# Optimization experiments

Hardware: AMD Instinct MI355X
Metric: run time of the kernel (lower is better)

## Reference

```python
import jax, jax.numpy as jnp
import numpy as np

B, T, KV = 128, 400, 128   # batch, encoder length, key/value size
V, E, H = 1024, 256, 512   # vocab, embed dim, decoder hidden dim
L = 300                    # decode length (train mode: y.shape[1])
SOS = 1                    # letter2index['<sos>'] (0 is padding_idx)
NEG = -1e9


def setup_inputs() -> dict:
    key = jax.random.key(0)
    ks = jax.random.split(key, 16)
    s1 = 1.0 / np.sqrt(H)   # torch LSTMCell init scale
    s2 = 1.0 / np.sqrt(KV)
    so = 1.0 / np.sqrt(2 * KV)
    emb = jax.random.normal(ks[4], (V, E), jnp.float32)
    emb = emb.at[0].set(0.0)  # padding_idx=0
    return {
        "enc_key": jax.random.normal(ks[0], (B, T, KV), jnp.float32),
        "enc_value": jax.random.normal(ks[1], (B, T, KV), jnp.float32),
        "encoder_len": jax.random.randint(ks[2], (B,), 1, T + 1),
        "y": jax.random.randint(ks[3], (B, L), 0, V),
        "embedding": emb,
        "w_ih1": jax.random.uniform(ks[5], (4 * H, KV + E), jnp.float32, -s1, s1),
        "w_hh1": jax.random.uniform(ks[6], (4 * H, H), jnp.float32, -s1, s1),
        "b_ih1": jax.random.uniform(ks[7], (4 * H,), jnp.float32, -s1, s1),
        "b_hh1": jax.random.uniform(ks[8], (4 * H,), jnp.float32, -s1, s1),
        "w_ih2": jax.random.uniform(ks[9], (4 * KV, H), jnp.float32, -s2, s2),
        "w_hh2": jax.random.uniform(ks[10], (4 * KV, KV), jnp.float32, -s2, s2),
        "b_ih2": jax.random.uniform(ks[11], (4 * KV,), jnp.float32, -s2, s2),
        "b_hh2": jax.random.uniform(ks[12], (4 * KV,), jnp.float32, -s2, s2),
        "w_out": jax.random.uniform(ks[13], (V, 2 * KV), jnp.float32, -so, so),
        "b_out": jax.random.uniform(ks[14], (V,), jnp.float32, -so, so),
    }


def _lstm_cell(x, h, c, w_ih, w_hh, b_ih, b_hh):
    gates = x @ w_ih.T + b_ih + h @ w_hh.T + b_hh
    i, f, g, o = jnp.split(gates, 4, axis=-1)
    c2 = jax.nn.sigmoid(f) * c + jax.nn.sigmoid(i) * jnp.tanh(g)
    h2 = jax.nn.sigmoid(o) * jnp.tanh(c2)
    return h2, c2


def reference(enc_key, enc_value, encoder_len, y, embedding,
              w_ih1, w_hh1, b_ih1, b_hh1,
              w_ih2, w_hh2, b_ih2, b_hh2,
              w_out, b_out):
    mask = jnp.arange(T)[None, :] < encoder_len[:, None]  # (B, T)

    # Teacher forcing (TF_rate -> 1): step 0 feeds <sos>, step i feeds y[:, i-1]
    char_emb = embedding[y]                               # (B, L, E)
    sos_emb = jnp.broadcast_to(embedding[SOS], (B, E))
    inputs = jnp.concatenate([sos_emb[:, None, :], char_emb[:, :-1, :]], axis=1)
    inputs = jnp.swapaxes(inputs, 0, 1)                   # (L, B, E)

    def step(carry, emb_t):
        h1, c1, h2, c2, context = carry
        x = jnp.concatenate([emb_t, context], axis=1)     # (B, E+KV)
        h1, c1 = _lstm_cell(x, h1, c1, w_ih1, w_hh1, b_ih1, b_hh1)
        h2, c2 = _lstm_cell(h1, h2, c2, w_ih2, w_hh2, b_ih2, b_hh2)
        query = h2                                        # (B, KV)
        energy = jnp.einsum('btd,bd->bt', enc_key, query)
        energy = jnp.where(mask, energy, NEG)
        attn = jax.nn.softmax(energy, axis=1)             # (B, T)
        context = jnp.einsum('bt,btd->bd', attn, enc_value)
        logits = jnp.concatenate([query, context], axis=1) @ w_out.T + b_out
        return (h1, c1, h2, c2, context), (logits, attn[0])

    zH = jnp.zeros((B, H), jnp.float32)
    zK = jnp.zeros((B, KV), jnp.float32)
    carry0 = (zH, zH, zK, zK, zK)
    _, (logits_seq, attn_plot) = jax.lax.scan(step, carry0, inputs)
    predictions = jnp.swapaxes(logits_seq, 0, 1)          # (B, L, V)
    return predictions, attn_plot                         # attn_plot: (L, T)
```

## Files before the change

### kernel.cpp

```cpp
#include <hip/hip_runtime.h>
#include <hip/hip_bf16.h>

#define BB   128
#define TT   400
#define KVD  128
#define VV   1024
#define EE   256
#define HH   512
#define LL   300
#define D1   896
#define NBLK 256
#define NTHR 256

#define XT_SZ   (D1 * BB)
#define XT_OFF  0
#define H2_SZ   (KVD * BB)
#define H2_OFF  (2 * XT_SZ)
#define FLAG_OFF (H2_OFF + 2 * H2_SZ)
#define PLOT_OFF (BB * LL * VV)

typedef unsigned short ushort_t;

__device__ __forceinline__ float bf2f(ushort_t u) {
  return __uint_as_float(((unsigned)u) << 16);
}
__device__ __forceinline__ ushort_t f2bf(float f) {
  unsigned u = __float_as_uint(f);
  return (ushort_t)((u + 0x7FFFu + ((u >> 16) & 1u)) >> 16);
}
__device__ __forceinline__ float sigm(float x) { return 1.0f / (1.0f + expf(-x)); }

__device__ __forceinline__ float ldx(const void* p, size_t i, bool isf) {
  return isf ? ((const float*)p)[i] : bf2f(((const ushort_t*)p)[i]);
}
__device__ __forceinline__ void stx(void* p, size_t i, float v, bool isf) {
  if (isf) ((float*)p)[i] = v; else ((ushort_t*)p)[i] = f2bf(v);
}

__global__ void probe_kernel(const void* __restrict__ w_out, float* __restrict__ ws) {
  if (blockIdx.x == 0 && threadIdx.x == 0) {
    const ushort_t* p = (const ushort_t*)w_out;
    int bad = 0;
    for (int i = 0; i < 512; ++i) {
      float v = bf2f(p[i]);
      if (!(fabsf(v) < 0.5f)) bad++;
    }
    unsigned* flags = (unsigned*)(ws + FLAG_OFF);
    flags[NBLK + 1] = (bad > 0) ? 1u : 0u;
  }
}

__global__ void __launch_bounds__(NTHR) init_kernel(const void* __restrict__ emb,
                                                    float* __restrict__ ws) {
  unsigned* flags = (unsigned*)(ws + FLAG_OFF);
  const bool isf = flags[NBLK + 1] != 0;
  int idx = blockIdx.x * NTHR + threadIdx.x;
  if (idx < XT_SZ) {
    int k = idx >> 7;
    ws[XT_OFF + idx] = (k < EE) ? ldx(emb, EE + k, isf) : 0.0f;
  }
  int j = idx - XT_SZ;
  if (j >= 0 && j < H2_SZ) ws[H2_OFF + j] = 0.0f;
  int f = idx - (XT_SZ + H2_SZ);
  if (f >= 0 && f < NBLK + 1) flags[f] = 0u;
}

__device__ __forceinline__ void grid_barrier(unsigned* flags, unsigned* gen, unsigned target) {
  __syncthreads();
  const int tid = threadIdx.x;
  if (blockIdx.x == 0) {
    if (tid > 0) {
      long spin = 0;
      while (__hip_atomic_load(&flags[tid], __ATOMIC_RELAXED, __HIP_MEMORY_SCOPE_AGENT) < target) {
        __builtin_amdgcn_s_sleep(2);
        if (++spin > (1L << 24)) break;
      }
    }
    __syncthreads();
    if (tid == 0) {
      __threadfence();
      __hip_atomic_store(gen, target, __ATOMIC_RELEASE, __HIP_MEMORY_SCOPE_AGENT);
    }
    __syncthreads();
  } else {
    if (tid == 0) {
      __threadfence();
      __hip_atomic_store(&flags[blockIdx.x], target, __ATOMIC_RELEASE, __HIP_MEMORY_SCOPE_AGENT);
      long spin = 0;
      while (__hip_atomic_load(gen, __ATOMIC_RELAXED, __HIP_MEMORY_SCOPE_AGENT) < target) {
        __builtin_amdgcn_s_sleep(2);
        if (++spin > (1L << 24)) break;
      }
      __threadfence();
    }
    __syncthreads();
  }
}

__global__ void __launch_bounds__(NTHR) decoder_kernel(
    const void* __restrict__ enc_key,
    const void* __restrict__ enc_value,
    const int*  __restrict__ enc_len,
    const int*  __restrict__ y,
    const void* __restrict__ emb,
    const void* __restrict__ w_ih1, const void* __restrict__ w_hh1,
    const void* __restrict__ b_ih1, const void* __restrict__ b_hh1,
    const void* __restrict__ w_ih2, const void* __restrict__ w_hh2,
    const void* __restrict__ b_ih2, const void* __restrict__ b_hh2,
    const void* __restrict__ w_out, const void* __restrict__ b_out,
    void* __restrict__ out, float* __restrict__ ws)
{
  __shared__ float sW1[8][D1];
  __shared__ float sW2[4][640];
  __shared__ float sWo[4][256];
  __shared__ float sB1[8];
  __shared__ float sB2[4];
  __shared__ float sBo[4];
  __shared__ float sRed[4];
  __shared__ float sAttn[TT];
  __shared__ float sH2[KVD];
  __shared__ float sGex[2][BB];

  const int tid = threadIdx.x;
  const int w   = blockIdx.x;
  unsigned* flags = (unsigned*)(ws + FLAG_OFF);
  unsigned* gen   = flags + NBLK;
  const bool isf  = flags[NBLK + 1] != 0;

  for (int i = tid; i < 8 * D1; i += NTHR) {
    int r = i / D1, k = i - r * D1;
    int g = r & 3, h = r >> 2;
    int R = g * HH + 2 * w + h;
    sW1[r][k] = (k < EE + KVD) ? ldx(w_ih1, (size_t)R * (EE + KVD) + k, isf)
                               : ldx(w_hh1, (size_t)R * HH + (k - (EE + KVD)), isf);
  }
  if (tid < 8) {
    int R = (tid & 3) * HH + 2 * w + (tid >> 2);
    sB1[tid] = ldx(b_ih1, R, isf) + ldx(b_hh1, R, isf);
  }
  if (w < BB) {
    for (int i = tid; i < 4 * 640; i += NTHR) {
      int g = i / 640, k = i - g * 640;
      int R = g * KVD + w;
      sW2[g][k] = (k < HH) ? ldx(w_ih2, (size_t)R * HH + k, isf)
                           : ldx(w_hh2, (size_t)R * KVD + (k - HH), isf);
    }
    if (tid < 4) {
      int R = tid * KVD + w;
      sB2[tid] = ldx(b_ih2, R, isf) + ldx(b_hh2, R, isf);
    }
  }
  for (int i = tid; i < 4 * 256; i += NTHR) {
    int r = i >> 8, d = i & 255;
    sWo[r][d] = ldx(w_out, (size_t)(4 * w + r) * 256 + d, isf);
  }
  if (tid < 4) sBo[tid] = ldx(b_out, 4 * w + tid, isf);
  __syncthreads();

  const int b  = tid & 127;
  const int hi = tid >> 7;
  float c1 = 0.0f;
  float c2 = 0.0f;

  unsigned target = 0;

  for (int t = 0; t <= LL; ++t) {
    const int p0 = t & 1;
    float* xT0  = ws + XT_OFF + p0 * XT_SZ;
    float* xT1  = ws + XT_OFF + (p0 ^ 1) * XT_SZ;
    float* h2T0 = ws + H2_OFF + p0 * H2_SZ;
    float* h2T1 = ws + H2_OFF + (p0 ^ 1) * H2_SZ;

    if (t > 0) {
      float a0 = sBo[2 * hi], a1 = sBo[2 * hi + 1];
      const float4* r0 = (const float4*)&sWo[2 * hi][0];
      const float4* r1 = (const float4*)&sWo[2 * hi + 1][0];
      const float* hp = h2T0 + b;
      #pragma unroll 4
      for (int q = 0; q < 32; ++q) {
        float x0 = hp[0], x1 = hp[BB], x2 = hp[2 * BB], x3 = hp[3 * BB]; hp += 4 * BB;
        float4 u0 = r0[q], u1 = r1[q];
        a0 += u0.x * x0 + u0.y * x1 + u0.z * x2 + u0.w * x3;
        a1 += u1.x * x0 + u1.y * x1 + u1.z * x2 + u1.w * x3;
      }
      const float* cp = xT0 + 256 * BB + b;
      #pragma unroll 4
      for (int q = 0; q < 32; ++q) {
        float x0 = cp[0], x1 = cp[BB], x2 = cp[2 * BB], x3 = cp[3 * BB]; cp += 4 * BB;
        float4 u0 = r0[32 + q], u1 = r1[32 + q];
        a0 += u0.x * x0 + u0.y * x1 + u0.z * x2 + u0.w * x3;
        a1 += u1.x * x0 + u1.y * x1 + u1.z * x2 + u1.w * x3;
      }
      int v = 4 * w + 2 * hi;
      size_t oidx = (size_t)b * (LL * VV) + (size_t)(t - 1) * VV + v;
      stx(out, oidx, a0, isf);
      stx(out, oidx + 1, a1, isf);
    }
    if (t == LL) break;

    {
      const int hu = 2 * w + hi;
      float a0 = sB1[4 * hi + 0], a1 = sB1[4 * hi + 1];
      float a2 = sB1[4 * hi + 2], a3 = sB1[4 * hi + 3];
      const float4* q0 = (const float4*)&sW1[4 * hi + 0][0];
      const float4* q1 = (const float4*)&sW1[4 * hi + 1][0];
      const float4* q2 = (const float4*)&sW1[4 * hi + 2][0];
      const float4* q3 = (const float4*)&sW1[4 * hi + 3][0];
      const float* xp = xT0 + b;
      #pragma unroll 2
      for (int q = 0; q < 224; ++q) {
        float x0 = xp[0], x1 = xp[BB], x2 = xp[2 * BB], x3 = xp[3 * BB]; xp += 4 * BB;
        float4 u0 = q0[q], u1 = q1[q], u2 = q2[q], u3 = q3[q];
        a0 += u0.x * x0 + u0.y * x1 + u0.z * x2 + u0.w * x3;
        a1 += u1.x * x0 + u1.y * x1 + u1.z * x2 + u1.w * x3;
        a2 += u2.x * x0 + u2.y * x1 + u2.z * x2 + u2.w * x3;
        a3 += u3.x * x0 + u3.y * x1 + u3.z * x2 + u3.w * x3;
      }
      float ig = sigm(a0), fg = sigm(a1), gg = tanhf(a2), og = sigm(a3);
      c1 = fg * c1 + ig * gg;
      float h1v = og * tanhf(c1);
      xT1[(384 + hu) * BB + b] = h1v;
    }
    grid_barrier(flags, gen, ++target);

    if (w < BB) {
      float a0 = sB2[2 * hi], a1 = sB2[2 * hi + 1];
      const float4* r0 = (const float4*)&sW2[2 * hi][0];
      const float4* r1 = (const float4*)&sW2[2 * hi + 1][0];
      const float* xp = xT1 + 384 * BB + b;
      #pragma unroll 4
      for (int q = 0; q < 128; ++q) {
        float x0 = xp[0], x1 = xp[BB], x2 = xp[2 * BB], x3 = xp[3 * BB]; xp += 4 * BB;
        float4 u0 = r0[q], u1 = r1[q];
        a0 += u0.x * x0 + u0.y * x1 + u0.z * x2 + u0.w * x3;
        a1 += u1.x * x0 + u1.y * x1 + u1.z * x2 + u1.w * x3;
      }
      const float* hp = h2T0 + b;
      #pragma unroll 4
      for (int q = 0; q < 32; ++q) {
        float x0 = hp[0], x1 = hp[BB], x2 = hp[2 * BB], x3 = hp[3 * BB]; hp += 4 * BB;
        float4 u0 = r0[128 + q], u1 = r1[128 + q];
        a0 += u0.x * x0 + u0.y * x1 + u0.z * x2 + u0.w * x3;
        a1 += u1.x * x0 + u1.y * x1 + u1.z * x2 + u1.w * x3;
      }
      if (hi == 1) { sGex[0][b] = tanhf(a0); sGex[1][b] = sigm(a1); }
      __syncthreads();
      if (hi == 0) {
        c2 = sigm(a1) * c2 + sigm(a0) * sGex[0][b];
        float h2v = sGex[1][b] * tanhf(c2);
        h2T1[w * BB + b] = h2v;
      }
    } else {
      int j = w - BB;
      int tok = y[j * LL + t];
      xT1[tid * BB + j] = ldx(emb, (size_t)tok * EE + tid, isf);
    }
    grid_barrier(flags, gen, ++target);

    if (w < BB) {
      const int rb = w;
      if (tid < KVD) sH2[tid] = h2T1[tid * BB + rb];
      __syncthreads();
      const int len = enc_len[rb];
      float lmax = -3.0e38f;
      #pragma unroll
      for (int rep = 0; rep < 2; ++rep) {
        int tp = tid + rep * 256;
        float e = -3.0e38f;
        if (tp < TT) {
          float acc = 0.0f;
          if (isf) {
            const float4* kr = (const float4*)((const float*)enc_key + ((size_t)rb * TT + tp) * KVD);
            #pragma unroll 8
            for (int q = 0; q < 32; ++q) {
              float4 u = kr[q];
              acc += u.x * sH2[4 * q + 0] + u.y * sH2[4 * q + 1]
                   + u.z * sH2[4 * q + 2] + u.w * sH2[4 * q + 3];
            }
          } else {
            const ushort4* kr = (const ushort4*)((const ushort_t*)enc_key + ((size_t)rb * TT + tp) * KVD);
            #pragma unroll 8
            for (int q = 0; q < 32; ++q) {
              ushort4 u = kr[q];
              acc += bf2f(u.x) * sH2[4 * q + 0] + bf2f(u.y) * sH2[4 * q + 1]
                   + bf2f(u.z) * sH2[4 * q + 2] + bf2f(u.w) * sH2[4 * q + 3];
            }
          }
          e = (tp < len) ? acc : -1e9f;
          sAttn[tp] = e;
        }
        lmax = fmaxf(lmax, e);
      }
      for (int off = 32; off > 0; off >>= 1) lmax = fmaxf(lmax, __shfl_down(lmax, off, 64));
      if ((tid & 63) == 0) sRed[tid >> 6] = lmax;
      __syncthreads();
      const float m = fmaxf(fmaxf(sRed[0], sRed[1]), fmaxf(sRed[2], sRed[3]));
      float lsum = 0.0f;
      #pragma unroll
      for (int rep = 0; rep < 2; ++rep) {
        int tp = tid + rep * 256;
        if (tp < TT) { float a = expf(sAttn[tp] - m); sAttn[tp] = a; lsum += a; }
      }
      for (int off = 32; off > 0; off >>= 1) lsum += __shfl_down(lsum, off, 64);
      __syncthreads();
      if ((tid & 63) == 0) sRed[tid >> 6] = lsum;
      __syncthreads();
      const float rS = 1.0f / (sRed[0] + sRed[1] + sRed[2] + sRed[3]);
      #pragma unroll
      for (int rep = 0; rep < 2; ++rep) {
        int tp = tid + rep * 256;
        if (tp < TT) {
          float a = sAttn[tp] * rS;
          sAttn[tp] = a;
          if (rb == 0) stx(out, (size_t)PLOT_OFF + (size_t)t * TT + tp, a, isf);
        }
      }
      __syncthreads();
      {
        const int d = tid & 127, half = tid >> 7;
        float acc = 0.0f;
        if (isf) {
          const float* vc = (const float*)enc_value + ((size_t)rb * TT + half * 200) * KVD + d;
          for (int tp2 = 0; tp2 < 200; ++tp2) acc += sAttn[half * 200 + tp2] * vc[(size_t)tp2 * KVD];
        } else {
          const ushort_t* vc = (const ushort_t*)enc_value + ((size_t)rb * TT + half * 200) * KVD + d;
          for (int tp2 = 0; tp2 < 200; ++tp2) acc += sAttn[half * 200 + tp2] * bf2f(vc[(size_t)tp2 * KVD]);
        }
        if (half == 1) sGex[0][d] = acc;
        __syncthreads();
        if (half == 0) xT1[(256 + d) * BB + rb] = acc + sGex[0][d];
      }
    }
    grid_barrier(flags, gen, ++target);
  }
}

extern "C" void kernel_launch(void* const* d_in, const int* in_sizes, int n_in,
                              void* d_out, int out_size, void* d_ws, size_t ws_size,
                              hipStream_t stream) {
  const void* enc_key   = d_in[0];
  const void* enc_value = d_in[1];
  const int*  enc_len   = (const int*)d_in[2];
  const int*  y         = (const int*)d_in[3];
  const void* emb       = d_in[4];
  const void* w_ih1     = d_in[5];
  const void* w_hh1     = d_in[6];
  const void* b_ih1     = d_in[7];
  const void* b_hh1     = d_in[8];
  const void* w_ih2     = d_in[9];
  const void* w_hh2     = d_in[10];
  const void* b_ih2     = d_in[11];
  const void* b_hh2     = d_in[12];
  const void* w_out     = d_in[13];
  const void* b_out     = d_in[14];
  float* ws = (float*)d_ws;

  probe_kernel<<<dim3(1), dim3(64), 0, stream>>>(w_out, ws);
  init_kernel<<<dim3((XT_SZ + H2_SZ + NBLK + 1 + NTHR - 1) / NTHR), dim3(NTHR), 0, stream>>>(emb, ws);
  decoder_kernel<<<dim3(NBLK), dim3(NTHR), 0, stream>>>(
      enc_key, enc_value, enc_len, y, emb,
      w_ih1, w_hh1, b_ih1, b_hh1,
      w_ih2, w_hh2, b_ih2, b_hh2,
      w_out, b_out, d_out, ws);
}
```

Baseline: 31.83 ms.

## Stage activation chunks through LDS with register prefetch in LSTM and output GEMVs

Replaces the direct strided global reads of the transposed activation vectors (x, h1, h2, context) with a double-step pipeline. Each block cooperatively loads 32-row chunks as coalesced float4 into registers, writes them to a shared buffer, and prefetches the next chunk while computing from LDS. The aim is to cut redundant per-thread global/L2 traffic, since both halves of the block read the same activations, and to hide load latency. In exchange it adds two __syncthreads per chunk and 16KB more shared memory.

```diff
diff --git a/kernel.cpp b/kernel.cpp
--- a/kernel.cpp
+++ b/kernel.cpp
@@ -96,6 +96,27 @@
     __syncthreads();
   }
 }
+
+#define STAGE_LOAD(PF, SRC4, C) \
+  { _Pragma("unroll") for (int j = 0; j < 4; ++j) PF[j] = (SRC4)[(size_t)(C) * 1024 + j * 256 + tid]; }
+#define STAGE_WRITE(PF) \
+  { float4* s4 = (float4*)sX; _Pragma("unroll") for (int j = 0; j < 4; ++j) s4[j * 256 + tid] = PF[j]; }
+#define CHUNK_CP4(WB) \
+  { _Pragma("unroll") for (int q = 0; q < 8; ++q) { \
+      float x0 = sX[(4*q+0)*128 + b], x1 = sX[(4*q+1)*128 + b]; \
+      float x2 = sX[(4*q+2)*128 + b], x3 = sX[(4*q+3)*128 + b]; \
+      float4 u0 = q0[(WB)+q], u1 = q1[(WB)+q], u2 = q2[(WB)+q], u3 = q3[(WB)+q]; \
+      a0 += u0.x*x0 + u0.y*x1 + u0.z*x2 + u0.w*x3; \
+      a1 += u1.x*x0 + u1.y*x1 + u1.z*x2 + u1.w*x3; \
+      a2 += u2.x*x0 + u2.y*x1 + u2.z*x2 + u2.w*x3; \
+      a3 += u3.x*x0 + u3.y*x1 + u3.z*x2 + u3.w*x3; } }
+#define CHUNK_CP2(WB) \
+  { _Pragma("unroll") for (int q = 0; q < 8; ++q) { \
+      float x0 = sX[(4*q+0)*128 + b], x1 = sX[(4*q+1)*128 + b]; \
+      float x2 = sX[(4*q+2)*128 + b], x3 = sX[(4*q+3)*128 + b]; \
+      float4 u0 = r0[(WB)+q], u1 = r1[(WB)+q]; \
+      a0 += u0.x*x0 + u0.y*x1 + u0.z*x2 + u0.w*x3; \
+      a1 += u1.x*x0 + u1.y*x1 + u1.z*x2 + u1.w*x3; } }
 
 __global__ void __launch_bounds__(NTHR) decoder_kernel(
     const void* __restrict__ enc_key,
@@ -120,6 +141,7 @@
   __shared__ float sAttn[TT];
   __shared__ float sH2[KVD];
   __shared__ float sGex[2][BB];
+  __shared__ float sX[32 * 128];
 
   const int tid = threadIdx.x;
   const int w   = blockIdx.x;
@@ -175,21 +197,19 @@
       float a0 = sBo[2 * hi], a1 = sBo[2 * hi + 1];
       const float4* r0 = (const float4*)&sWo[2 * hi][0];
       const float4* r1 = (const float4*)&sWo[2 * hi + 1][0];
-      const float* hp = h2T0 + b;
-      #pragma unroll 4
-      for (int q = 0; q < 32; ++q) {
-        float x0 = hp[0], x1 = hp[BB], x2 = hp[2 * BB], x3 = hp[3 * BB]; hp += 4 * BB;
-        float4 u0 = r0[q], u1 = r1[q];
-        a0 += u0.x * x0 + u0.y * x1 + u0.z * x2 + u0.w * x3;
-        a1 += u1.x * x0 + u1.y * x1 + u1.z * x2 + u1.w * x3;
-      }
-      const float* cp = xT0 + 256 * BB + b;
-      #pragma unroll 4
-      for (int q = 0; q < 32; ++q) {
-        float x0 = cp[0], x1 = cp[BB], x2 = cp[2 * BB], x3 = cp[3 * BB]; cp += 4 * BB;
-        float4 u0 = r0[32 + q], u1 = r1[32 + q];
-        a0 += u0.x * x0 + u0.y * x1 + u0.z * x2 + u0.w * x3;
-        a1 += u1.x * x0 + u1.y * x1 + u1.z * x2 + u1.w * x3;
+      const float4* hsrc = (const float4*)h2T0;
+      const float4* csrc = (const float4*)(xT0 + 256 * BB);
+      float4 pf[4];
+      STAGE_LOAD(pf, hsrc, 0)
+      for (int c = 0; c < 8; ++c) {
+        __syncthreads();
+        STAGE_WRITE(pf)
+        if (c < 7) {
+          if (c < 3) STAGE_LOAD(pf, hsrc, c + 1)
+          else       STAGE_LOAD(pf, csrc, c - 3)
+        }
+        __syncthreads();
+        CHUNK_CP2(c * 8)
       }
       int v = 4 * w + 2 * hi;
       size_t oidx = (size_t)b * (LL * VV) + (size_t)(t - 1) * VV + v;
@@ -206,15 +226,15 @@
       const float4* q1 = (const float4*)&sW1[4 * hi + 1][0];
       const float4* q2 = (const float4*)&sW1[4 * hi + 2][0];
       const float4* q3 = (const float4*)&sW1[4 * hi + 3][0];
-      const float* xp = xT0 + b;
-      #pragma unroll 2
-      for (int q = 0; q < 224; ++q) {
-        float x0 = xp[0], x1 = xp[BB], x2 = xp[2 * BB], x3 = xp[3 * BB]; xp += 4 * BB;
-        float4 u0 = q0[q], u1 = q1[q], u2 = q2[q], u3 = q3[q];
-        a0 += u0.x * x0 + u0.y * x1 + u0.z * x2 + u0.w * x3;
-        a1 += u1.x * x0 + u1.y * x1 + u1.z * x2 + u1.w * x3;
-        a2 += u2.x * x0 + u2.y * x1 + u2.z * x2 + u2.w * x3;
-        a3 += u3.x * x0 + u3.y * x1 + u3.z * x2 + u3.w * x3;
+      const float4* xsrc = (const float4*)xT0;
+      float4 pf[4];
+      STAGE_LOAD(pf, xsrc, 0)
+      for (int c = 0; c < 28; ++c) {
+        __syncthreads();
+        STAGE_WRITE(pf)
+        if (c < 27) STAGE_LOAD(pf, xsrc, c + 1)
+        __syncthreads();
+        CHUNK_CP4(c * 8)
       }
       float ig = sigm(a0), fg = sigm(a1), gg = tanhf(a2), og = sigm(a3);
       c1 = fg * c1 + ig * gg;
@@ -227,21 +247,19 @@
       float a0 = sB2[2 * hi], a1 = sB2[2 * hi + 1];
       const float4* r0 = (const float4*)&sW2[2 * hi][0];
       const float4* r1 = (const float4*)&sW2[2 * hi + 1][0];
-      const float* xp = xT1 + 384 * BB + b;
-      #pragma unroll 4
-      for (int q = 0; q < 128; ++q) {
-        float x0 = xp[0], x1 = xp[BB], x2 = xp[2 * BB], x3 = xp[3 * BB]; xp += 4 * BB;
-        float4 u0 = r0[q], u1 = r1[q];
-        a0 += u0.x * x0 + u0.y * x1 + u0.z * x2 + u0.w * x3;
-        a1 += u1.x * x0 + u1.y * x1 + u1.z * x2 + u1.w * x3;
-      }
-      const float* hp = h2T0 + b;
-      #pragma unroll 4
-      for (int q = 0; q < 32; ++q) {
-        float x0 = hp[0], x1 = hp[BB], x2 = hp[2 * BB], x3 = hp[3 * BB]; hp += 4 * BB;
-        float4 u0 = r0[128 + q], u1 = r1[128 + q];
-        a0 += u0.x * x0 + u0.y * x1 + u0.z * x2 + u0.w * x3;
-        a1 += u1.x * x0 + u1.y * x1 + u1.z * x2 + u1.w * x3;
+      const float4* xsrc = (const float4*)(xT1 + 384 * BB);
+      const float4* hsrc = (const float4*)h2T0;
+      float4 pf[4];
+      STAGE_LOAD(pf, xsrc, 0)
+      for (int c = 0; c < 20; ++c) {
+        __syncthreads();
+        STAGE_WRITE(pf)
+        if (c < 19) {
+          if (c < 15) STAGE_LOAD(pf, xsrc, c + 1)
+          else        STAGE_LOAD(pf, hsrc, c - 15)
+        }
+        __syncthreads();
+        CHUNK_CP2(c * 8)
       }
       if (hi == 1) { sGex[0][b] = tanhf(a0); sGex[1][b] = sigm(a1); }
       __syncthreads();
```

Measured after the change: 50.33 ms. 1.58x slower.

## Switch activation buffers to batch-major layout and split accumulators for ILP

Applied to the files above, without the earlier changes.

Transposes the shared workspace activations (xT, h2T) from feature-major to batch-major so each thread reads its own row with float4 vector loads instead of strided scalar loads. All matvec loops are also split into two independent accumulator chains, and the attention-context loop uses two partial sums, to expose more instruction-level parallelism. The trade-off is that adjacent threads now read addresses a full row apart, so global loads are no longer coalesced across lanes, and the writes of h1/h2/context become scattered.

```diff
diff --git a/kernel.cpp b/kernel.cpp
--- a/kernel.cpp
+++ b/kernel.cpp
@@ -56,7 +56,7 @@
   const bool isf = flags[NBLK + 1] != 0;
   int idx = blockIdx.x * NTHR + threadIdx.x;
   if (idx < XT_SZ) {
-    int k = idx >> 7;
+    int k = idx % D1;
     ws[XT_OFF + idx] = (k < EE) ? ldx(emb, EE + k, isf) : 0.0f;
   }
   int j = idx - XT_SZ;
@@ -173,24 +173,22 @@
 
     if (t > 0) {
       float a0 = sBo[2 * hi], a1 = sBo[2 * hi + 1];
+      float e0 = 0.0f, e1 = 0.0f;
       const float4* r0 = (const float4*)&sWo[2 * hi][0];
       const float4* r1 = (const float4*)&sWo[2 * hi + 1][0];
-      const float* hp = h2T0 + b;
-      #pragma unroll 4
+      const float4* hp4 = (const float4*)(h2T0 + (size_t)b * KVD);
+      const float4* cp4 = (const float4*)(xT0 + (size_t)b * D1 + 256);
+      #pragma unroll 2
       for (int q = 0; q < 32; ++q) {
-        float x0 = hp[0], x1 = hp[BB], x2 = hp[2 * BB], x3 = hp[3 * BB]; hp += 4 * BB;
-        float4 u0 = r0[q], u1 = r1[q];
-        a0 += u0.x * x0 + u0.y * x1 + u0.z * x2 + u0.w * x3;
-        a1 += u1.x * x0 + u1.y * x1 + u1.z * x2 + u1.w * x3;
-      }
-      const float* cp = xT0 + 256 * BB + b;
-      #pragma unroll 4
-      for (int q = 0; q < 32; ++q) {
-        float x0 = cp[0], x1 = cp[BB], x2 = cp[2 * BB], x3 = cp[3 * BB]; cp += 4 * BB;
-        float4 u0 = r0[32 + q], u1 = r1[32 + q];
-        a0 += u0.x * x0 + u0.y * x1 + u0.z * x2 + u0.w * x3;
-        a1 += u1.x * x0 + u1.y * x1 + u1.z * x2 + u1.w * x3;
-      }
+        float4 xA = hp4[q], xB = cp4[q];
+        float4 uA0 = r0[q], uA1 = r1[q];
+        float4 uB0 = r0[32 + q], uB1 = r1[32 + q];
+        a0 += uA0.x * xA.x + uA0.y * xA.y + uA0.z * xA.z + uA0.w * xA.w;
+        a1 += uA1.x * xA.x + uA1.y * xA.y + uA1.z * xA.z + uA1.w * xA.w;
+        e0 += uB0.x * xB.x + uB0.y * xB.y + uB0.z * xB.z + uB0.w * xB.w;
+        e1 += uB1.x * xB.x + uB1.y * xB.y + uB1.z * xB.z + uB1.w * xB.w;
+      }
+      a0 += e0; a1 += e1;
       int v = 4 * w + 2 * hi;
       size_t oidx = (size_t)b * (LL * VV) + (size_t)(t - 1) * VV + v;
       stx(out, oidx, a0, isf);
@@ -202,64 +200,76 @@
       const int hu = 2 * w + hi;
       float a0 = sB1[4 * hi + 0], a1 = sB1[4 * hi + 1];
       float a2 = sB1[4 * hi + 2], a3 = sB1[4 * hi + 3];
+      float e0 = 0.0f, e1 = 0.0f, e2 = 0.0f, e3 = 0.0f;
       const float4* q0 = (const float4*)&sW1[4 * hi + 0][0];
       const float4* q1 = (const float4*)&sW1[4 * hi + 1][0];
       const float4* q2 = (const float4*)&sW1[4 * hi + 2][0];
       const float4* q3 = (const float4*)&sW1[4 * hi + 3][0];
-      const float* xp = xT0 + b;
+      const float4* xp4 = (const float4*)(xT0 + (size_t)b * D1);
       #pragma unroll 2
-      for (int q = 0; q < 224; ++q) {
-        float x0 = xp[0], x1 = xp[BB], x2 = xp[2 * BB], x3 = xp[3 * BB]; xp += 4 * BB;
-        float4 u0 = q0[q], u1 = q1[q], u2 = q2[q], u3 = q3[q];
-        a0 += u0.x * x0 + u0.y * x1 + u0.z * x2 + u0.w * x3;
-        a1 += u1.x * x0 + u1.y * x1 + u1.z * x2 + u1.w * x3;
-        a2 += u2.x * x0 + u2.y * x1 + u2.z * x2 + u2.w * x3;
-        a3 += u3.x * x0 + u3.y * x1 + u3.z * x2 + u3.w * x3;
-      }
+      for (int q = 0; q < 112; ++q) {
+        float4 xA = xp4[q], xB = xp4[112 + q];
+        float4 uA0 = q0[q], uA1 = q1[q], uA2 = q2[q], uA3 = q3[q];
+        float4 uB0 = q0[112 + q], uB1 = q1[112 + q], uB2 = q2[112 + q], uB3 = q3[112 + q];
+        a0 += uA0.x * xA.x + uA0.y * xA.y + uA0.z * xA.z + uA0.w * xA.w;
+        a1 += uA1.x * xA.x + uA1.y * xA.y + uA1.z * xA.z + uA1.w * xA.w;
+        a2 += uA2.x * xA.x + uA2.y * xA.y + uA2.z * xA.z + uA2.w * xA.w;
+        a3 += uA3.x * xA.x + uA3.y * xA.y + uA3.z * xA.z + uA3.w * xA.w;
+        e0 += uB0.x * xB.x + uB0.y * xB.y + uB0.z * xB.z + uB0.w * xB.w;
+        e1 += uB1.x * xB.x + uB1.y * xB.y + uB1.z * xB.z + uB1.w * xB.w;
+        e2 += uB2.x * xB.x + uB2.y * xB.y + uB2.z * xB.z + uB2.w * xB.w;
+        e3 += uB3.x * xB.x + uB3.y * xB.y + uB3.z * xB.z + uB3.w * xB.w;
+      }
+      a0 += e0; a1 += e1; a2 += e2; a3 += e3;
       float ig = sigm(a0), fg = sigm(a1), gg = tanhf(a2), og = sigm(a3);
       c1 = fg * c1 + ig * gg;
       float h1v = og * tanhf(c1);
-      xT1[(384 + hu) * BB + b] = h1v;
+      xT1[(size_t)b * D1 + 384 + hu] = h1v;
     }
     grid_barrier(flags, gen, ++target);
 
     if (w < BB) {
       float a0 = sB2[2 * hi], a1 = sB2[2 * hi + 1];
+      float e0 = 0.0f, e1 = 0.0f;
       const float4* r0 = (const float4*)&sW2[2 * hi][0];
       const float4* r1 = (const float4*)&sW2[2 * hi + 1][0];
-      const float* xp = xT1 + 384 * BB + b;
-      #pragma unroll 4
-      for (int q = 0; q < 128; ++q) {
-        float x0 = xp[0], x1 = xp[BB], x2 = xp[2 * BB], x3 = xp[3 * BB]; xp += 4 * BB;
-        float4 u0 = r0[q], u1 = r1[q];
-        a0 += u0.x * x0 + u0.y * x1 + u0.z * x2 + u0.w * x3;
-        a1 += u1.x * x0 + u1.y * x1 + u1.z * x2 + u1.w * x3;
-      }
-      const float* hp = h2T0 + b;
+      const float4* xp4 = (const float4*)(xT1 + (size_t)b * D1 + 384);
+      #pragma unroll 2
+      for (int q = 0; q < 64; ++q) {
+        float4 xA = xp4[q], xB = xp4[64 + q];
+        float4 uA0 = r0[q], uA1 = r1[q];
+        float4 uB0 = r0[64 + q], uB1 = r1[64 + q];
+        a0 += uA0.x * xA.x + uA0.y * xA.y + uA0.z * xA.z + uA0.w * xA.w;
+        a1 += uA1.x * xA.x + uA1.y * xA.y + uA1.z * xA.z + uA1.w * xA.w;
+        e0 += uB0.x * xB.x + uB0.y * xB.y + uB0.z * xB.z + uB0.w * xB.w;
+        e1 += uB1.x * xB.x + uB1.y * xB.y + uB1.z * xB.z + uB1.w * xB.w;
+      }
+      a0 += e0; a1 += e1;
+      const float4* hp4 = (const float4*)(h2T0 + (size_t)b * KVD);
       #pragma unroll 4
       for (int q = 0; q < 32; ++q) {
-        float x0 = hp[0], x1 = hp[BB], x2 = hp[2 * BB], x3 = hp[3 * BB]; hp += 4 * BB;
+        float4 x = hp4[q];
         float4 u0 = r0[128 + q], u1 = r1[128 + q];
-        a0 += u0.x * x0 + u0.y * x1 + u0.z * x2 + u0.w * x3;
-        a1 += u1.x * x0 + u1.y * x1 + u1.z * x2 + u1.w * x3;
+        a0 += u0.x * x.x + u0.y * x.y + u0.z * x.z + u0.w * x.w;
+        a1 += u1.x * x.x + u1.y * x.y + u1.z * x.z + u1.w * x.w;
       }
       if (hi == 1) { sGex[0][b] = tanhf(a0); sGex[1][b] = sigm(a1); }
       __syncthreads();
       if (hi == 0) {
         c2 = sigm(a1) * c2 + sigm(a0) * sGex[0][b];
         float h2v = sGex[1][b] * tanhf(c2);
-        h2T1[w * BB + b] = h2v;
+        h2T1[(size_t)b * KVD + w] = h2v;
       }
     } else {
       int j = w - BB;
       int tok = y[j * LL + t];
-      xT1[tid * BB + j] = ldx(emb, (size_t)tok * EE + tid, isf);
+      xT1[(size_t)j * D1 + tid] = ldx(emb, (size_t)tok * EE + tid, isf);
     }
     grid_barrier(flags, gen, ++target);
 
     if (w < BB) {
       const int rb = w;
-      if (tid < KVD) sH2[tid] = h2T1[tid * BB + rb];
+      if (tid < KVD) sH2[tid] = h2T1[(size_t)rb * KVD + tid];
       __syncthreads();
       const int len = enc_len[rb];
       float lmax = -3.0e38f;
@@ -318,17 +328,29 @@
       __syncthreads();
       {
         const int d = tid & 127, half = tid >> 7;
-        float acc = 0.0f;
+        const int tb = half * 200;
+        float accA = 0.0f, accB = 0.0f;
         if (isf) {
-          const float* vc = (const float*)enc_value + ((size_t)rb * TT + half * 200) * KVD + d;
-          for (int tp2 = 0; tp2 < 200; ++tp2) acc += sAttn[half * 200 + tp2] * vc[(size_t)tp2 * KVD];
+          const float* vcA = (const float*)enc_value + ((size_t)rb * TT + tb) * KVD + d;
+          const float* vcB = vcA + (size_t)100 * KVD;
+          #pragma unroll 4
+          for (int tp2 = 0; tp2 < 100; ++tp2) {
+            accA += sAttn[tb + tp2] * vcA[(size_t)tp2 * KVD];
+            accB += sAttn[tb + 100 + tp2] * vcB[(size_t)tp2 * KVD];
+          }
         } else {
-          const ushort_t* vc = (const ushort_t*)enc_value + ((size_t)rb * TT + half * 200) * KVD + d;
-          for (int tp2 = 0; tp2 < 200; ++tp2) acc += sAttn[half * 200 + tp2] * bf2f(vc[(size_t)tp2 * KVD]);
+          const ushort_t* vcA = (const ushort_t*)enc_value + ((size_t)rb * TT + tb) * KVD + d;
+          const ushort_t* vcB = vcA + (size_t)100 * KVD;
+          #pragma unroll 4
+          for (int tp2 = 0; tp2 < 100; ++tp2) {
+            accA += sAttn[tb + tp2] * bf2f(vcA[(size_t)tp2 * KVD]);
+            accB += sAttn[tb + 100 + tp2] * bf2f(vcB[(size_t)tp2 * KVD]);
+          }
         }
+        float acc = accA + accB;
         if (half == 1) sGex[0][d] = acc;
         __syncthreads();
-        if (half == 0) xT1[(256 + d) * BB + rb] = acc + sGex[0][d];
+        if (half == 0) xT1[(size_t)rb * D1 + 256 + d] = acc + sGex[0][d];
       }
     }
     grid_barrier(flags, gen, ++target);
```

Result: slower. 34.88 ms (+9.6%).
